# Kernel tuning notes

Hardware: AMD Instinct MI355X
Metric: run time of the kernel (lower is better)

## Reference

```python
import jax, jax.numpy as jnp
import numpy as np

B, L, H, N_OUT = 16, 2048, 256, 12
CODEBOOK_VALUE = 1.0


def setup_inputs() -> dict:
    key = jax.random.key(0)
    ks = jax.random.split(key, 7)
    s = 1.0 / np.sqrt(H)  # PyTorch default U(-1/sqrt(H), 1/sqrt(H)) init
    return {
        "embedding": jax.random.normal(ks[0], (B, L, H), jnp.float32),
        # nn.GRU(1, H): weight_ih_l0 is [3H, 1] -> store as vector [3H]
        "w_ih": jax.random.uniform(ks[1], (3 * H,), jnp.float32, -s, s),
        "w_hh": jax.random.uniform(ks[2], (3 * H, H), jnp.float32, -s, s),
        "b_ih": jax.random.uniform(ks[3], (3 * H,), jnp.float32, -s, s),
        "b_hh": jax.random.uniform(ks[4], (3 * H,), jnp.float32, -s, s),
        # nn.Linear(H, 1)
        "w_out": jax.random.uniform(ks[5], (H,), jnp.float32, -s, s),
        "b_out": jax.random.uniform(ks[6], (1,), jnp.float32, -s, s),
    }


def reference(embedding, w_ih, w_hh, b_ih, b_hh, w_out, b_out):
    Bv, Lv, Hv = embedding.shape
    e = embedding.reshape(Bv * Lv, Hv)  # [BL, H]; every step adds e to hidden

    def step(carry, _):
        h, x = carry                      # h: [BL, H], x: [BL] (quantized feedback)
        h_in = h + e                      # hidden fed to GRU is hidden_state + embedding
        # input dim is 1, so W_ih @ x reduces to outer product x * w_ih
        gi = x[:, None] * w_ih[None, :] + b_ih          # [BL, 3H]
        gh = h_in @ w_hh.T + b_hh                        # [BL, 3H]
        gi_r, gi_z, gi_n = jnp.split(gi, 3, axis=-1)     # PyTorch gate order: r, z, n
        gh_r, gh_z, gh_n = jnp.split(gh, 3, axis=-1)
        r = jax.nn.sigmoid(gi_r + gh_r)
        z = jax.nn.sigmoid(gi_z + gh_z)
        n = jnp.tanh(gi_n + r * gh_n)
        h_new = (1.0 - z) * n + z * h_in                 # GRU cell update
        o = h_new @ w_out + b_out[0]                     # [BL] output_layer
        q = jnp.where(o > 0, CODEBOOK_VALUE, -CODEBOOK_VALUE)
        return (h_new, q), (o, q)

    h0 = jnp.zeros_like(e)
    x0 = jnp.zeros((e.shape[0],), e.dtype)
    _, (outs, qs) = jax.lax.scan(step, (h0, x0), None, length=N_OUT)
    # outs/qs: [N_OUT, BL] -> [B, L, N_OUT]
    outputs = jnp.transpose(outs).reshape(Bv, Lv, N_OUT)
    quantized = jnp.transpose(qs).reshape(Bv, Lv, N_OUT)
    return outputs, quantized
```

## Files before the change

kernel.cpp:

```cpp
#include <hip/hip_runtime.h>
#include <math.h>

namespace {
constexpr int kBL = 16 * 2048;
constexpr int kH = 256;
constexpr int kNOut = 12;
constexpr int kRows = 64;
constexpr int kThreads = 1024;
constexpr int kS = 264;
constexpr int kWhh = 3 * kH * kH;
}

using short8 = __attribute__((ext_vector_type(8))) short;
using f32x4 = __attribute__((ext_vector_type(4))) float;

__device__ inline void bsplit(float v, short& h, short& l) {
  unsigned u = __float_as_uint(v);
  unsigned rh = u + 0x7FFFu + ((u >> 16) & 1u);
  h = (short)(rh >> 16);
  float hf = __uint_as_float(rh & 0xFFFF0000u);
  float r = v - hf;
  unsigned u2 = __float_as_uint(r);
  unsigned rl = u2 + 0x7FFFu + ((u2 >> 16) & 1u);
  l = (short)(rl >> 16);
}

__global__ void split_whh_kernel(const float* __restrict__ w,
                                 short* __restrict__ hi, short* __restrict__ lo) {
  const int i = (blockIdx.x * 256 + threadIdx.x) * 4;
  const float4 v = *reinterpret_cast<const float4*>(w + i);
  short4 h4, l4;
  bsplit(v.x, h4.x, l4.x);
  bsplit(v.y, h4.y, l4.y);
  bsplit(v.z, h4.z, l4.z);
  bsplit(v.w, h4.w, l4.w);
  *reinterpret_cast<short4*>(hi + i) = h4;
  *reinterpret_cast<short4*>(lo + i) = l4;
}

#define MFMA(A, B, C) __builtin_amdgcn_mfma_f32_16x16x32_bf16((A), (B), (C), 0, 0, 0)

__global__ __launch_bounds__(kThreads, 4)
void rbq_mfma3_kernel(const float* __restrict__ emb,
                      const float* __restrict__ w_ih,
                      const float* __restrict__ b_ih,
                      const float* __restrict__ b_hh,
                      const float* __restrict__ w_out,
                      const float* __restrict__ b_out,
                      const short* __restrict__ Bh,
                      const short* __restrict__ Bl,
                      float* __restrict__ out) {
  __shared__ short Ah[kRows][kS];
  __shared__ short Al[kRows][kS];
  __shared__ float osc[kRows][17];
  __shared__ float xq[kRows];

  const int tid = threadIdx.x;
  const int lane = tid & 63;
  const int wv = __builtin_amdgcn_readfirstlane(tid >> 6);
  const int grp = lane >> 4;
  const int c16 = lane & 15;
  const int row0 = blockIdx.x * kRows;
  const int j = wv * 16 + c16;

  const float wihr = w_ih[j], wihz = w_ih[kH + j], wihn = w_ih[2 * kH + j];
  const float bihr = b_ih[j], bihz = b_ih[kH + j], bihn = b_ih[2 * kH + j];
  const float bhhr = b_hh[j], bhhz = b_hh[kH + j], bhhn = b_hh[2 * kH + j];
  const float wo = w_out[j];
  const float bo = b_out[0];
  const size_t q_off = (size_t)kBL * kNOut;

  float h_reg[4][4];
#pragma unroll
  for (int m = 0; m < 4; ++m)
#pragma unroll
    for (int r = 0; r < 4; ++r) {
      const int rl = m * 16 + grp * 4 + r;
      const float e = emb[(size_t)(row0 + rl) * kH + j];
      h_reg[m][r] = e;
      short hh, hl;
      bsplit(e, hh, hl);
      Ah[rl][j] = hh;
      Al[rl][j] = hl;
    }
  if (tid < kRows) xq[tid] = 0.0f;
  __syncthreads();

  for (int step = 0; step < kNOut; ++step) {
    f32x4 acc[4][3];
#pragma unroll
    for (int m = 0; m < 4; ++m) {
      acc[m][0] = f32x4{bhhr, bhhr, bhhr, bhhr};
      acc[m][1] = f32x4{bhhz, bhhz, bhhz, bhhz};
      acc[m][2] = f32x4{bhhn, bhhn, bhhn, bhhn};
    }

#pragma unroll 1
    for (int kc = 0; kc < 8; ++kc) {
      const int ko = kc * 32 + grp * 8;
      short8 bh[3], bl[3];
#pragma unroll
      for (int g = 0; g < 3; ++g) {
        const size_t base = (size_t)(g * kH + j) * kH + ko;
        bh[g] = *reinterpret_cast<const short8*>(Bh + base);
        bl[g] = *reinterpret_cast<const short8*>(Bl + base);
      }
#pragma unroll
      for (int m = 0; m < 4; ++m) {
        const short8 ah = *reinterpret_cast<const short8*>(&Ah[m * 16 + c16][ko]);
        const short8 al = *reinterpret_cast<const short8*>(&Al[m * 16 + c16][ko]);
#pragma unroll
        for (int g = 0; g < 3; ++g) acc[m][g] = MFMA(ah, bh[g], acc[m][g]);
#pragma unroll
        for (int g = 0; g < 3; ++g) acc[m][g] = MFMA(al, bh[g], acc[m][g]);
#pragma unroll
        for (int g = 0; g < 3; ++g) acc[m][g] = MFMA(ah, bl[g], acc[m][g]);
      }
    }
    __syncthreads();

    float opart[4][4];
#pragma unroll
    for (int m = 0; m < 4; ++m) {
#pragma unroll
      for (int r = 0; r < 4; ++r) {
        const int rl = m * 16 + grp * 4 + r;
        const float x = xq[rl];
        const float ghr = acc[m][0][r];
        const float ghz = acc[m][1][r];
        const float ghn = acc[m][2][r];
        const float gr = fmaf(x, wihr, bihr) + ghr;
        const float gz = fmaf(x, wihz, bihz) + ghz;
        const float gni = fmaf(x, wihn, bihn);
        const float rg = 1.0f / (1.0f + __expf(-gr));
        const float zg = 1.0f / (1.0f + __expf(-gz));
        const float ta = gni + rg * ghn;
        const float at = fabsf(ta);
        const float et = __expf(-2.0f * at);
        const float th = copysignf((1.0f - et) / (1.0f + et), ta);
        const float hn = fmaf(zg, h_reg[m][r] - th, th);
        opart[m][r] = hn * wo;
        const float hnext = hn + emb[(size_t)(row0 + rl) * kH + j];
        h_reg[m][r] = hnext;
        short hh, hl;
        bsplit(hnext, hh, hl);
        Ah[rl][j] = hh;
        Al[rl][j] = hl;
      }
    }

#pragma unroll
    for (int m = 0; m < 4; ++m)
#pragma unroll
      for (int r = 0; r < 4; ++r) {
#pragma unroll
        for (int mask = 1; mask < 16; mask <<= 1)
          opart[m][r] += __shfl_xor(opart[m][r], mask, 16);
      }
    if (c16 == 0) {
#pragma unroll
      for (int m = 0; m < 4; ++m)
#pragma unroll
        for (int r = 0; r < 4; ++r)
          osc[m * 16 + grp * 4 + r][wv] = opart[m][r];
    }
    __syncthreads();

    if (tid < kRows) {
      float s = bo;
#pragma unroll
      for (int w2 = 0; w2 < 16; ++w2) s += osc[tid][w2];
      const float q = s > 0.0f ? 1.0f : -1.0f;
      const size_t gr = (size_t)(row0 + tid);
      out[gr * kNOut + step] = s;
      out[q_off + gr * kNOut + step] = q;
      xq[tid] = q;
    }
  }
}

extern "C" void kernel_launch(void* const* d_in, const int* in_sizes, int n_in,
                              void* d_out, int out_size, void* d_ws, size_t ws_size,
                              hipStream_t stream) {
  (void)in_sizes; (void)n_in; (void)out_size; (void)ws_size;
  const float* emb = (const float*)d_in[0];
  const float* w_ih = (const float*)d_in[1];
  const float* w_hh = (const float*)d_in[2];
  const float* b_ih = (const float*)d_in[3];
  const float* b_hh = (const float*)d_in[4];
  const float* w_out = (const float*)d_in[5];
  const float* b_out = (const float*)d_in[6];

  short* Bh = (short*)d_ws;
  short* Bl = Bh + kWhh;

  split_whh_kernel<<<kWhh / (256 * 4), 256, 0, stream>>>(w_hh, Bh, Bl);
  rbq_mfma3_kernel<<<kBL / kRows, kThreads, 0, stream>>>(
      emb, w_ih, b_ih, b_hh, w_out, b_out, Bh, Bl, (float*)d_out);
}
```

Baseline: 738.5 us.

## Double-buffer hidden-state LDS tiles to drop a barrier and broadcast feedback via shuffles

Splits the bf16 hi/lo hidden-state tiles into two ping-pong buffers. Each step then writes the next hidden state into the other buffer, which removes the barrier between the MFMA loop and the gate update. Every wave now computes the output reduction redundantly and keeps the quantized feedback in a register, read back with __shfl, so the xq shared array and one serialized tid<64 section go away. It also raises wave priority around the MFMA loop. The cost is doubled LDS usage per block, which may cut the number of resident blocks, plus redundant reduction work in every wave.

```diff
diff --git a/kernel.cpp b/kernel.cpp
--- a/kernel.cpp
+++ b/kernel.cpp
@@ -41,7 +41,7 @@
 #define MFMA(A, B, C) __builtin_amdgcn_mfma_f32_16x16x32_bf16((A), (B), (C), 0, 0, 0)
 
 __global__ __launch_bounds__(kThreads, 4)
-void rbq_mfma3_kernel(const float* __restrict__ emb,
+void rbq_mfma4_kernel(const float* __restrict__ emb,
                       const float* __restrict__ w_ih,
                       const float* __restrict__ b_ih,
                       const float* __restrict__ b_hh,
@@ -50,10 +50,9 @@
                       const short* __restrict__ Bh,
                       const short* __restrict__ Bl,
                       float* __restrict__ out) {
-  __shared__ short Ah[kRows][kS];
-  __shared__ short Al[kRows][kS];
-  __shared__ float osc[kRows][17];
-  __shared__ float xq[kRows];
+  __shared__ short Ah[2][kRows][kS];
+  __shared__ short Al[2][kRows][kS];
+  __shared__ float osc[kRows][16];
 
   const int tid = threadIdx.x;
   const int lane = tid & 63;
@@ -80,12 +79,13 @@
       h_reg[m][r] = e;
       short hh, hl;
       bsplit(e, hh, hl);
-      Ah[rl][j] = hh;
-      Al[rl][j] = hl;
-    }
-  if (tid < kRows) xq[tid] = 0.0f;
+      Ah[0][rl][j] = hh;
+      Al[0][rl][j] = hl;
+    }
+  float xqr = 0.0f;
   __syncthreads();
 
+  int p = 0;
   for (int step = 0; step < kNOut; ++step) {
     f32x4 acc[4][3];
 #pragma unroll
@@ -95,6 +95,7 @@
       acc[m][2] = f32x4{bhhn, bhhn, bhhn, bhhn};
     }
 
+    __builtin_amdgcn_s_setprio(1);
 #pragma unroll 1
     for (int kc = 0; kc < 8; ++kc) {
       const int ko = kc * 32 + grp * 8;
@@ -107,8 +108,8 @@
       }
 #pragma unroll
       for (int m = 0; m < 4; ++m) {
-        const short8 ah = *reinterpret_cast<const short8*>(&Ah[m * 16 + c16][ko]);
-        const short8 al = *reinterpret_cast<const short8*>(&Al[m * 16 + c16][ko]);
+        const short8 ah = *reinterpret_cast<const short8*>(&Ah[p][m * 16 + c16][ko]);
+        const short8 al = *reinterpret_cast<const short8*>(&Al[p][m * 16 + c16][ko]);
 #pragma unroll
         for (int g = 0; g < 3; ++g) acc[m][g] = MFMA(ah, bh[g], acc[m][g]);
 #pragma unroll
@@ -117,7 +118,7 @@
         for (int g = 0; g < 3; ++g) acc[m][g] = MFMA(ah, bl[g], acc[m][g]);
       }
     }
-    __syncthreads();
+    __builtin_amdgcn_s_setprio(0);
 
     float opart[4][4];
 #pragma unroll
@@ -125,7 +126,7 @@
 #pragma unroll
       for (int r = 0; r < 4; ++r) {
         const int rl = m * 16 + grp * 4 + r;
-        const float x = xq[rl];
+        const float x = __shfl(xqr, rl);
         const float ghr = acc[m][0][r];
         const float ghz = acc[m][1][r];
         const float ghn = acc[m][2][r];
@@ -144,8 +145,8 @@
         h_reg[m][r] = hnext;
         short hh, hl;
         bsplit(hnext, hh, hl);
-        Ah[rl][j] = hh;
-        Al[rl][j] = hl;
+        Ah[p ^ 1][rl][j] = hh;
+        Al[p ^ 1][rl][j] = hl;
       }
     }
 
@@ -166,16 +167,25 @@
     }
     __syncthreads();
 
-    if (tid < kRows) {
+    {
+      const float4 o0 = *reinterpret_cast<const float4*>(&osc[lane][0]);
+      const float4 o1 = *reinterpret_cast<const float4*>(&osc[lane][4]);
+      const float4 o2 = *reinterpret_cast<const float4*>(&osc[lane][8]);
+      const float4 o3 = *reinterpret_cast<const float4*>(&osc[lane][12]);
       float s = bo;
-#pragma unroll
-      for (int w2 = 0; w2 < 16; ++w2) s += osc[tid][w2];
+      s += o0.x; s += o0.y; s += o0.z; s += o0.w;
+      s += o1.x; s += o1.y; s += o1.z; s += o1.w;
+      s += o2.x; s += o2.y; s += o2.z; s += o2.w;
+      s += o3.x; s += o3.y; s += o3.z; s += o3.w;
       const float q = s > 0.0f ? 1.0f : -1.0f;
-      const size_t gr = (size_t)(row0 + tid);
-      out[gr * kNOut + step] = s;
-      out[q_off + gr * kNOut + step] = q;
-      xq[tid] = q;
-    }
+      xqr = q;
+      if (wv == 0) {
+        const size_t gr = (size_t)(row0 + lane);
+        out[gr * kNOut + step] = s;
+        out[q_off + gr * kNOut + step] = q;
+      }
+    }
+    p ^= 1;
   }
 }
 
@@ -195,6 +205,6 @@
   short* Bl = Bh + kWhh;
 
   split_whh_kernel<<<kWhh / (256 * 4), 256, 0, stream>>>(w_hh, Bh, Bl);
-  rbq_mfma3_kernel<<<kBL / kRows, kThreads, 0, stream>>>(
+  rbq_mfma4_kernel<<<kBL / kRows, kThreads, 0, stream>>>(
       emb, w_ih, b_ih, b_hh, w_out, b_out, Bh, Bl, (float*)d_out);
 }
```

Measured after the change: 784.2 us. +6.2%, slower.

## Software-pipeline GRU halves: overlap gate math of one half with MFMAs of other

Applied to the files above, without the earlier changes.

Halves the block to 512 threads, with each wave owning 32 hidden columns instead of 16. The 64 rows are split into two halves, and the gate nonlinearity for one half is interleaved with the MFMA matmul for the other, using double-buffered accumulators. The quantized feedback moves from shared memory into a register broadcast by shuffle, and output finalization folds into the next phase. The aim is to hide the serial gate and elementwise phase behind matrix-core work, at the cost of higher register pressure, fewer waves per block and more complex synchronization.

```diff
diff --git a/kernel.cpp b/kernel.cpp
--- a/kernel.cpp
+++ b/kernel.cpp
@@ -6,7 +6,7 @@
 constexpr int kH = 256;
 constexpr int kNOut = 12;
 constexpr int kRows = 64;
-constexpr int kThreads = 1024;
+constexpr int kThreads = 512;
 constexpr int kS = 264;
 constexpr int kWhh = 3 * kH * kH;
 }
@@ -40,8 +40,8 @@
 
 #define MFMA(A, B, C) __builtin_amdgcn_mfma_f32_16x16x32_bf16((A), (B), (C), 0, 0, 0)
 
-__global__ __launch_bounds__(kThreads, 4)
-void rbq_mfma3_kernel(const float* __restrict__ emb,
+__global__ __launch_bounds__(kThreads, 2)
+void rbq_mfma5_kernel(const float* __restrict__ emb,
                       const float* __restrict__ w_ih,
                       const float* __restrict__ b_ih,
                       const float* __restrict__ b_hh,
@@ -53,7 +53,6 @@
   __shared__ short Ah[kRows][kS];
   __shared__ short Al[kRows][kS];
   __shared__ float osc[kRows][17];
-  __shared__ float xq[kRows];
 
   const int tid = threadIdx.x;
   const int lane = tid & 63;
@@ -61,120 +60,188 @@
   const int grp = lane >> 4;
   const int c16 = lane & 15;
   const int row0 = blockIdx.x * kRows;
-  const int j = wv * 16 + c16;
-
-  const float wihr = w_ih[j], wihz = w_ih[kH + j], wihn = w_ih[2 * kH + j];
-  const float bihr = b_ih[j], bihz = b_ih[kH + j], bihn = b_ih[2 * kH + j];
-  const float bhhr = b_hh[j], bhhz = b_hh[kH + j], bhhn = b_hh[2 * kH + j];
-  const float wo = w_out[j];
+
+  float wihr[2], wihz[2], wihn[2], bihr[2], bihz[2], bihn[2];
+  float bhhr[2], bhhz[2], bhhn[2], wo[2];
+#pragma unroll
+  for (int t = 0; t < 2; ++t) {
+    const int j = wv * 32 + t * 16 + c16;
+    wihr[t] = w_ih[j]; wihz[t] = w_ih[kH + j]; wihn[t] = w_ih[2 * kH + j];
+    bihr[t] = b_ih[j]; bihz[t] = b_ih[kH + j]; bihn[t] = b_ih[2 * kH + j];
+    bhhr[t] = b_hh[j]; bhhz[t] = b_hh[kH + j]; bhhn[t] = b_hh[2 * kH + j];
+    wo[t] = w_out[j];
+  }
   const float bo = b_out[0];
   const size_t q_off = (size_t)kBL * kNOut;
 
-  float h_reg[4][4];
-#pragma unroll
-  for (int m = 0; m < 4; ++m)
-#pragma unroll
-    for (int r = 0; r < 4; ++r) {
-      const int rl = m * 16 + grp * 4 + r;
-      const float e = emb[(size_t)(row0 + rl) * kH + j];
-      h_reg[m][r] = e;
-      short hh, hl;
-      bsplit(e, hh, hl);
-      Ah[rl][j] = hh;
-      Al[rl][j] = hl;
-    }
-  if (tid < kRows) xq[tid] = 0.0f;
+  float h_reg0[2][4][2];
+  float h_reg1[2][4][2];
+#pragma unroll
+  for (int mt = 0; mt < 4; ++mt)
+#pragma unroll
+    for (int r = 0; r < 4; ++r)
+#pragma unroll
+      for (int t = 0; t < 2; ++t) {
+        const int rl = mt * 16 + grp * 4 + r;
+        const int j = wv * 32 + t * 16 + c16;
+        const float e = emb[(size_t)(row0 + rl) * kH + j];
+        if (mt < 2) h_reg0[mt][r][t] = e; else h_reg1[mt - 2][r][t] = e;
+        short hh, hl;
+        bsplit(e, hh, hl);
+        Ah[rl][j] = hh;
+        Al[rl][j] = hl;
+      }
+  float xqr = 0.0f;
   __syncthreads();
 
-  for (int step = 0; step < kNOut; ++step) {
-    f32x4 acc[4][3];
-#pragma unroll
-    for (int m = 0; m < 4; ++m) {
-      acc[m][0] = f32x4{bhhr, bhhr, bhhr, bhhr};
-      acc[m][1] = f32x4{bhhz, bhhz, bhhz, bhhz};
-      acc[m][2] = f32x4{bhhn, bhhn, bhhn, bhhn};
-    }
-
-#pragma unroll 1
+  f32x4 accA[2][2][3];
+  f32x4 accB[2][2][3];
+
+  auto phase = [&](f32x4 (&accC)[2][2][3], f32x4 (&accN)[2][2][3],
+                   float (&hreg)[2][4][2], const int mtC0, const int mtB0,
+                   const int qlo, const int outStep, const bool build,
+                   const bool gates, const bool fin) {
+    if (fin) {
+      float s = bo;
+#pragma unroll
+      for (int w2 = 0; w2 < 16; ++w2) s += osc[lane][w2];
+      const float qn = s > 0.0f ? 1.0f : -1.0f;
+      const bool inh = (lane >> 5) == (qlo >> 5);
+      xqr = inh ? qn : xqr;
+      if (wv == 0 && inh) {
+        const size_t gr = (size_t)(row0 + lane);
+        out[gr * kNOut + outStep] = s;
+        out[q_off + gr * kNOut + outStep] = qn;
+      }
+    }
+    if (build) {
+#pragma unroll
+      for (int m2 = 0; m2 < 2; ++m2)
+#pragma unroll
+        for (int t = 0; t < 2; ++t) {
+          accN[m2][t][0] = f32x4{bhhr[t], bhhr[t], bhhr[t], bhhr[t]};
+          accN[m2][t][1] = f32x4{bhhz[t], bhhz[t], bhhz[t], bhhz[t]};
+          accN[m2][t][2] = f32x4{bhhn[t], bhhn[t], bhhn[t], bhhn[t]};
+        }
+    }
+    float opart[2][4][2];
+
+    auto gate = [&](const int m2, const int r, const int t, const int rl,
+                    const float ev) {
+      const float x = __shfl(xqr, rl);
+      const float ghr = accC[m2][t][0][r];
+      const float ghz = accC[m2][t][1][r];
+      const float ghn = accC[m2][t][2][r];
+      const float gr = fmaf(x, wihr[t], bihr[t]) + ghr;
+      const float gz = fmaf(x, wihz[t], bihz[t]) + ghz;
+      const float gni = fmaf(x, wihn[t], bihn[t]);
+      const float rg = 1.0f / (1.0f + __expf(-gr));
+      const float zg = 1.0f / (1.0f + __expf(-gz));
+      const float ta = gni + rg * ghn;
+      const float at = fabsf(ta);
+      const float et = __expf(-2.0f * at);
+      const float th = copysignf((1.0f - et) / (1.0f + et), ta);
+      const float hn = fmaf(zg, hreg[m2][r][t] - th, th);
+      opart[m2][r][t] = hn * wo[t];
+      const float hnext = hn + ev;
+      hreg[m2][r][t] = hnext;
+      short hh, hl2;
+      bsplit(hnext, hh, hl2);
+      const int jj = wv * 32 + t * 16 + c16;
+      Ah[rl][jj] = hh;
+      Al[rl][jj] = hl2;
+    };
+
+#pragma unroll
     for (int kc = 0; kc < 8; ++kc) {
       const int ko = kc * 32 + grp * 8;
-      short8 bh[3], bl[3];
-#pragma unroll
-      for (int g = 0; g < 3; ++g) {
-        const size_t base = (size_t)(g * kH + j) * kH + ko;
-        bh[g] = *reinterpret_cast<const short8*>(Bh + base);
-        bl[g] = *reinterpret_cast<const short8*>(Bl + base);
-      }
-#pragma unroll
-      for (int m = 0; m < 4; ++m) {
-        const short8 ah = *reinterpret_cast<const short8*>(&Ah[m * 16 + c16][ko]);
-        const short8 al = *reinterpret_cast<const short8*>(&Al[m * 16 + c16][ko]);
-#pragma unroll
-        for (int g = 0; g < 3; ++g) acc[m][g] = MFMA(ah, bh[g], acc[m][g]);
-#pragma unroll
-        for (int g = 0; g < 3; ++g) acc[m][g] = MFMA(al, bh[g], acc[m][g]);
-#pragma unroll
-        for (int g = 0; g < 3; ++g) acc[m][g] = MFMA(ah, bl[g], acc[m][g]);
-      }
-    }
+      const int m2u = kc >> 2, ru = kc & 3;
+      const int rlu = (mtC0 + m2u) * 16 + grp * 4 + ru;
+      float e0 = 0.f, e1 = 0.f;
+      if (gates) {
+        e0 = emb[(size_t)(row0 + rlu) * kH + wv * 32 + c16];
+        e1 = emb[(size_t)(row0 + rlu) * kH + wv * 32 + 16 + c16];
+      }
+      short8 ah[2], al[2], bh[2][3], bl[2][3];
+      if (build) {
+#pragma unroll
+        for (int t = 0; t < 2; ++t)
+#pragma unroll
+          for (int g = 0; g < 3; ++g) {
+            const size_t base =
+                (size_t)(g * kH + wv * 32 + t * 16 + c16) * kH + ko;
+            bh[t][g] = *reinterpret_cast<const short8*>(Bh + base);
+            bl[t][g] = *reinterpret_cast<const short8*>(Bl + base);
+          }
+#pragma unroll
+        for (int m2 = 0; m2 < 2; ++m2) {
+          ah[m2] = *reinterpret_cast<const short8*>(&Ah[(mtB0 + m2) * 16 + c16][ko]);
+          al[m2] = *reinterpret_cast<const short8*>(&Al[(mtB0 + m2) * 16 + c16][ko]);
+        }
+#pragma unroll
+        for (int m2 = 0; m2 < 2; ++m2)
+#pragma unroll
+          for (int g = 0; g < 3; ++g) {
+            accN[m2][0][g] = MFMA(ah[m2], bh[0][g], accN[m2][0][g]);
+            accN[m2][0][g] = MFMA(al[m2], bh[0][g], accN[m2][0][g]);
+            accN[m2][0][g] = MFMA(ah[m2], bl[0][g], accN[m2][0][g]);
+          }
+      }
+      if (gates) gate(m2u, ru, 0, rlu, e0);
+      if (build) {
+#pragma unroll
+        for (int m2 = 0; m2 < 2; ++m2)
+#pragma unroll
+          for (int g = 0; g < 3; ++g) {
+            accN[m2][1][g] = MFMA(ah[m2], bh[1][g], accN[m2][1][g]);
+            accN[m2][1][g] = MFMA(al[m2], bh[1][g], accN[m2][1][g]);
+            accN[m2][1][g] = MFMA(ah[m2], bl[1][g], accN[m2][1][g]);
+          }
+      }
+      if (gates) gate(m2u, ru, 1, rlu, e1);
+    }
+
+    if (gates) {
+#pragma unroll
+      for (int m2 = 0; m2 < 2; ++m2)
+#pragma unroll
+        for (int r = 0; r < 4; ++r)
+#pragma unroll
+          for (int t = 0; t < 2; ++t) {
+#pragma unroll
+            for (int mask = 1; mask < 16; mask <<= 1)
+              opart[m2][r][t] += __shfl_xor(opart[m2][r][t], mask, 16);
+          }
+      if (c16 == 0) {
+#pragma unroll
+        for (int m2 = 0; m2 < 2; ++m2)
+#pragma unroll
+          for (int r = 0; r < 4; ++r)
+#pragma unroll
+            for (int t = 0; t < 2; ++t)
+              osc[(mtC0 + m2) * 16 + grp * 4 + r][2 * wv + t] = opart[m2][r][t];
+      }
+    }
+  };
+
+  phase(accB, accA, h_reg0, 0, 0, 0, 0, true, false, false);
+
+  for (int step = 0; step < kNOut; ++step) {
+    phase(accA, accB, h_reg0, 0, 2, 32, step - 1, true, true, step > 0);
     __syncthreads();
-
-    float opart[4][4];
-#pragma unroll
-    for (int m = 0; m < 4; ++m) {
-#pragma unroll
-      for (int r = 0; r < 4; ++r) {
-        const int rl = m * 16 + grp * 4 + r;
-        const float x = xq[rl];
-        const float ghr = acc[m][0][r];
-        const float ghz = acc[m][1][r];
-        const float ghn = acc[m][2][r];
-        const float gr = fmaf(x, wihr, bihr) + ghr;
-        const float gz = fmaf(x, wihz, bihz) + ghz;
-        const float gni = fmaf(x, wihn, bihn);
-        const float rg = 1.0f / (1.0f + __expf(-gr));
-        const float zg = 1.0f / (1.0f + __expf(-gz));
-        const float ta = gni + rg * ghn;
-        const float at = fabsf(ta);
-        const float et = __expf(-2.0f * at);
-        const float th = copysignf((1.0f - et) / (1.0f + et), ta);
-        const float hn = fmaf(zg, h_reg[m][r] - th, th);
-        opart[m][r] = hn * wo;
-        const float hnext = hn + emb[(size_t)(row0 + rl) * kH + j];
-        h_reg[m][r] = hnext;
-        short hh, hl;
-        bsplit(hnext, hh, hl);
-        Ah[rl][j] = hh;
-        Al[rl][j] = hl;
-      }
-    }
-
-#pragma unroll
-    for (int m = 0; m < 4; ++m)
-#pragma unroll
-      for (int r = 0; r < 4; ++r) {
-#pragma unroll
-        for (int mask = 1; mask < 16; mask <<= 1)
-          opart[m][r] += __shfl_xor(opart[m][r], mask, 16);
-      }
-    if (c16 == 0) {
-#pragma unroll
-      for (int m = 0; m < 4; ++m)
-#pragma unroll
-        for (int r = 0; r < 4; ++r)
-          osc[m * 16 + grp * 4 + r][wv] = opart[m][r];
-    }
+    phase(accB, accA, h_reg1, 2, 0, 0, step, step < kNOut - 1, true, true);
     __syncthreads();
-
-    if (tid < kRows) {
-      float s = bo;
-#pragma unroll
-      for (int w2 = 0; w2 < 16; ++w2) s += osc[tid][w2];
-      const float q = s > 0.0f ? 1.0f : -1.0f;
-      const size_t gr = (size_t)(row0 + tid);
-      out[gr * kNOut + step] = s;
-      out[q_off + gr * kNOut + step] = q;
-      xq[tid] = q;
+  }
+
+  {
+    float s = bo;
+#pragma unroll
+    for (int w2 = 0; w2 < 16; ++w2) s += osc[lane][w2];
+    const float qn = s > 0.0f ? 1.0f : -1.0f;
+    if (wv == 0 && lane >= 32) {
+      const size_t gr = (size_t)(row0 + lane);
+      out[gr * kNOut + (kNOut - 1)] = s;
+      out[q_off + gr * kNOut + (kNOut - 1)] = qn;
     }
   }
 }
@@ -195,6 +262,6 @@
   short* Bl = Bh + kWhh;
 
   split_whh_kernel<<<kWhh / (256 * 4), 256, 0, stream>>>(w_hh, Bh, Bl);
-  rbq_mfma3_kernel<<<kBL / kRows, kThreads, 0, stream>>>(
+  rbq_mfma5_kernel<<<kBL / kRows, kThreads, 0, stream>>>(
       emb, w_ih, b_ih, b_hh, w_out, b_out, Bh, Bl, (float*)d_out);
 }
```

Result: slower. 1.745 ms (+136.3%).

## Ping-pong two half-block warp groups to overlap MFMA and gate phases

Applied to the files above, without the earlier changes.

Splits each 1024-thread block into two 8-wave groups, each owning 32 rows. The groups alternate, so one runs the MFMA matmul while the other runs the gate math and output reduction. Gate parameters move to shared memory, the quantized feedback is kept in registers and broadcast with shuffles, and the MFMA phase raises wave priority. The aim is to hide the serial gate and reduction phase behind tensor-core work. In exchange, each wave now loads twice as many W_hh fragments per output row and the synchronisation schedule is more complex.

```diff
diff --git a/kernel.cpp b/kernel.cpp
--- a/kernel.cpp
+++ b/kernel.cpp
@@ -5,7 +5,6 @@
 constexpr int kBL = 16 * 2048;
 constexpr int kH = 256;
 constexpr int kNOut = 12;
-constexpr int kRows = 64;
 constexpr int kThreads = 1024;
 constexpr int kS = 264;
 constexpr int kWhh = 3 * kH * kH;
@@ -41,142 +40,201 @@
 #define MFMA(A, B, C) __builtin_amdgcn_mfma_f32_16x16x32_bf16((A), (B), (C), 0, 0, 0)
 
 __global__ __launch_bounds__(kThreads, 4)
-void rbq_mfma3_kernel(const float* __restrict__ emb,
-                      const float* __restrict__ w_ih,
-                      const float* __restrict__ b_ih,
-                      const float* __restrict__ b_hh,
-                      const float* __restrict__ w_out,
-                      const float* __restrict__ b_out,
-                      const short* __restrict__ Bh,
-                      const short* __restrict__ Bl,
-                      float* __restrict__ out) {
-  __shared__ short Ah[kRows][kS];
-  __shared__ short Al[kRows][kS];
-  __shared__ float osc[kRows][17];
-  __shared__ float xq[kRows];
+void rbq_pp_kernel(const float* __restrict__ emb,
+                   const float* __restrict__ w_ih,
+                   const float* __restrict__ b_ih,
+                   const float* __restrict__ b_hh,
+                   const float* __restrict__ w_out,
+                   const float* __restrict__ b_out,
+                   const short* __restrict__ Bh,
+                   const short* __restrict__ Bl,
+                   float* __restrict__ out) {
+  __shared__ short Ah[2][32][kS];
+  __shared__ short Al[2][32][kS];
+  __shared__ float prm[10][kH];
+  __shared__ float osc[2][32][12];
 
   const int tid = threadIdx.x;
   const int lane = tid & 63;
   const int wv = __builtin_amdgcn_readfirstlane(tid >> 6);
+  const int gid = wv >> 3;
+  const int gwv = wv & 7;
   const int grp = lane >> 4;
   const int c16 = lane & 15;
-  const int row0 = blockIdx.x * kRows;
-  const int j = wv * 16 + c16;
-
-  const float wihr = w_ih[j], wihz = w_ih[kH + j], wihn = w_ih[2 * kH + j];
-  const float bihr = b_ih[j], bihz = b_ih[kH + j], bihn = b_ih[2 * kH + j];
-  const float bhhr = b_hh[j], bhhz = b_hh[kH + j], bhhn = b_hh[2 * kH + j];
-  const float wo = w_out[j];
+  const int row0 = blockIdx.x * 64 + gid * 32;
+  const size_t q_off = (size_t)kBL * kNOut;
   const float bo = b_out[0];
-  const size_t q_off = (size_t)kBL * kNOut;
-
-  float h_reg[4][4];
-#pragma unroll
-  for (int m = 0; m < 4; ++m)
-#pragma unroll
-    for (int r = 0; r < 4; ++r) {
-      const int rl = m * 16 + grp * 4 + r;
-      const float e = emb[(size_t)(row0 + rl) * kH + j];
-      h_reg[m][r] = e;
-      short hh, hl;
-      bsplit(e, hh, hl);
-      Ah[rl][j] = hh;
-      Al[rl][j] = hl;
-    }
-  if (tid < kRows) xq[tid] = 0.0f;
+
+  if (tid < kH) {
+    const int u = tid;
+    prm[0][u] = w_ih[u];
+    prm[1][u] = w_ih[kH + u];
+    prm[2][u] = w_ih[2 * kH + u];
+    prm[3][u] = b_ih[u];
+    prm[4][u] = b_ih[kH + u];
+    prm[5][u] = b_ih[2 * kH + u];
+    prm[6][u] = b_hh[u];
+    prm[7][u] = b_hh[kH + u];
+    prm[8][u] = b_hh[2 * kH + u];
+    prm[9][u] = w_out[u];
+  }
+
+  float h_reg[2][4][2];
+  float xqr = 0.0f;
+#pragma unroll
+  for (int m = 0; m < 2; ++m)
+#pragma unroll
+    for (int r = 0; r < 4; ++r)
+#pragma unroll
+      for (int t = 0; t < 2; ++t) {
+        const int rl = m * 16 + grp * 4 + r;
+        const int j = gwv * 32 + t * 16 + c16;
+        const float e = emb[(size_t)(row0 + rl) * kH + j];
+        h_reg[m][r][t] = e;
+        short hh, hl;
+        bsplit(e, hh, hl);
+        Ah[gid][rl][j] = hh;
+        Al[gid][rl][j] = hl;
+      }
   __syncthreads();
 
-  for (int step = 0; step < kNOut; ++step) {
-    f32x4 acc[4][3];
-#pragma unroll
-    for (int m = 0; m < 4; ++m) {
-      acc[m][0] = f32x4{bhhr, bhhr, bhhr, bhhr};
-      acc[m][1] = f32x4{bhhz, bhhz, bhhz, bhhz};
-      acc[m][2] = f32x4{bhhn, bhhn, bhhn, bhhn};
-    }
-
+  f32x4 acc[2][2][3];
+
+  auto mfma_phase = [&]() {
+#pragma unroll
+    for (int t = 0; t < 2; ++t) {
+      const int j = gwv * 32 + t * 16 + c16;
+      const float br_ = prm[6][j], bz_ = prm[7][j], bn_ = prm[8][j];
+#pragma unroll
+      for (int m = 0; m < 2; ++m) {
+        acc[m][t][0] = f32x4{br_, br_, br_, br_};
+        acc[m][t][1] = f32x4{bz_, bz_, bz_, bz_};
+        acc[m][t][2] = f32x4{bn_, bn_, bn_, bn_};
+      }
+    }
+    __builtin_amdgcn_s_setprio(1);
 #pragma unroll 1
     for (int kc = 0; kc < 8; ++kc) {
       const int ko = kc * 32 + grp * 8;
-      short8 bh[3], bl[3];
-#pragma unroll
-      for (int g = 0; g < 3; ++g) {
-        const size_t base = (size_t)(g * kH + j) * kH + ko;
-        bh[g] = *reinterpret_cast<const short8*>(Bh + base);
-        bl[g] = *reinterpret_cast<const short8*>(Bl + base);
-      }
-#pragma unroll
-      for (int m = 0; m < 4; ++m) {
-        const short8 ah = *reinterpret_cast<const short8*>(&Ah[m * 16 + c16][ko]);
-        const short8 al = *reinterpret_cast<const short8*>(&Al[m * 16 + c16][ko]);
-#pragma unroll
-        for (int g = 0; g < 3; ++g) acc[m][g] = MFMA(ah, bh[g], acc[m][g]);
-#pragma unroll
-        for (int g = 0; g < 3; ++g) acc[m][g] = MFMA(al, bh[g], acc[m][g]);
-#pragma unroll
-        for (int g = 0; g < 3; ++g) acc[m][g] = MFMA(ah, bl[g], acc[m][g]);
-      }
-    }
-    __syncthreads();
-
-    float opart[4][4];
-#pragma unroll
-    for (int m = 0; m < 4; ++m) {
+      const short8 ah0 = *reinterpret_cast<const short8*>(&Ah[gid][c16][ko]);
+      const short8 al0 = *reinterpret_cast<const short8*>(&Al[gid][c16][ko]);
+      const short8 ah1 = *reinterpret_cast<const short8*>(&Ah[gid][16 + c16][ko]);
+      const short8 al1 = *reinterpret_cast<const short8*>(&Al[gid][16 + c16][ko]);
+#pragma unroll
+      for (int t = 0; t < 2; ++t) {
+        const int j = gwv * 32 + t * 16 + c16;
+        short8 bh[3], bl[3];
+#pragma unroll
+        for (int g = 0; g < 3; ++g) {
+          const size_t base = (size_t)(g * kH + j) * kH + ko;
+          bh[g] = *reinterpret_cast<const short8*>(Bh + base);
+          bl[g] = *reinterpret_cast<const short8*>(Bl + base);
+        }
+#pragma unroll
+        for (int g = 0; g < 3; ++g) {
+          acc[0][t][g] = MFMA(ah0, bh[g], acc[0][t][g]);
+          acc[1][t][g] = MFMA(ah1, bh[g], acc[1][t][g]);
+        }
+#pragma unroll
+        for (int g = 0; g < 3; ++g) {
+          acc[0][t][g] = MFMA(al0, bh[g], acc[0][t][g]);
+          acc[1][t][g] = MFMA(al1, bh[g], acc[1][t][g]);
+        }
+#pragma unroll
+        for (int g = 0; g < 3; ++g) {
+          acc[0][t][g] = MFMA(ah0, bl[g], acc[0][t][g]);
+          acc[1][t][g] = MFMA(ah1, bl[g], acc[1][t][g]);
+        }
+      }
+    }
+    __builtin_amdgcn_s_setprio(0);
+  };
+
+  auto gate_phase = [&]() {
+    float wr[2], wz[2], wn[2], br[2], bz[2], bn[2], wo[2];
+#pragma unroll
+    for (int t = 0; t < 2; ++t) {
+      const int j = gwv * 32 + t * 16 + c16;
+      wr[t] = prm[0][j]; wz[t] = prm[1][j]; wn[t] = prm[2][j];
+      br[t] = prm[3][j]; bz[t] = prm[4][j]; bn[t] = prm[5][j];
+      wo[t] = prm[9][j];
+    }
+    float opart[2][4];
+#pragma unroll
+    for (int m = 0; m < 2; ++m) {
 #pragma unroll
       for (int r = 0; r < 4; ++r) {
         const int rl = m * 16 + grp * 4 + r;
-        const float x = xq[rl];
-        const float ghr = acc[m][0][r];
-        const float ghz = acc[m][1][r];
-        const float ghn = acc[m][2][r];
-        const float gr = fmaf(x, wihr, bihr) + ghr;
-        const float gz = fmaf(x, wihz, bihz) + ghz;
-        const float gni = fmaf(x, wihn, bihn);
-        const float rg = 1.0f / (1.0f + __expf(-gr));
-        const float zg = 1.0f / (1.0f + __expf(-gz));
-        const float ta = gni + rg * ghn;
-        const float at = fabsf(ta);
-        const float et = __expf(-2.0f * at);
-        const float th = copysignf((1.0f - et) / (1.0f + et), ta);
-        const float hn = fmaf(zg, h_reg[m][r] - th, th);
-        opart[m][r] = hn * wo;
-        const float hnext = hn + emb[(size_t)(row0 + rl) * kH + j];
-        h_reg[m][r] = hnext;
-        short hh, hl;
-        bsplit(hnext, hh, hl);
-        Ah[rl][j] = hh;
-        Al[rl][j] = hl;
-      }
-    }
-
-#pragma unroll
-    for (int m = 0; m < 4; ++m)
-#pragma unroll
-      for (int r = 0; r < 4; ++r) {
+        const float x = __shfl(xqr, rl);
+#pragma unroll
+        for (int t = 0; t < 2; ++t) {
+          const int j = gwv * 32 + t * 16 + c16;
+          const float ghr = acc[m][t][0][r];
+          const float ghz = acc[m][t][1][r];
+          const float ghn = acc[m][t][2][r];
+          const float gr = fmaf(x, wr[t], br[t]) + ghr;
+          const float gz = fmaf(x, wz[t], bz[t]) + ghz;
+          const float gni = fmaf(x, wn[t], bn[t]);
+          const float rg = 1.0f / (1.0f + __expf(-gr));
+          const float zg = 1.0f / (1.0f + __expf(-gz));
+          const float ta = gni + rg * ghn;
+          const float at = fabsf(ta);
+          const float et = __expf(-2.0f * at);
+          const float th = copysignf((1.0f - et) / (1.0f + et), ta);
+          const float hn = fmaf(zg, h_reg[m][r][t] - th, th);
+          if (t == 0) opart[m][r] = hn * wo[0];
+          else opart[m][r] = fmaf(hn, wo[1], opart[m][r]);
+          const float hnext = hn + emb[(size_t)(row0 + rl) * kH + j];
+          h_reg[m][r][t] = hnext;
+          short hh, hl;
+          bsplit(hnext, hh, hl);
+          Ah[gid][rl][j] = hh;
+          Al[gid][rl][j] = hl;
+        }
 #pragma unroll
         for (int mask = 1; mask < 16; mask <<= 1)
           opart[m][r] += __shfl_xor(opart[m][r], mask, 16);
       }
+    }
     if (c16 == 0) {
 #pragma unroll
-      for (int m = 0; m < 4; ++m)
+      for (int m = 0; m < 2; ++m)
 #pragma unroll
         for (int r = 0; r < 4; ++r)
-          osc[m * 16 + grp * 4 + r][wv] = opart[m][r];
-    }
+          osc[gid][m * 16 + grp * 4 + r][gwv] = opart[m][r];
+    }
+  };
+
+  auto fin = [&](const int step) {
+    const int row = lane & 31;
+    const f32x4 s0 = *reinterpret_cast<const f32x4*>(&osc[gid][row][0]);
+    const f32x4 s1 = *reinterpret_cast<const f32x4*>(&osc[gid][row][4]);
+    float s = bo;
+    s += s0[0]; s += s0[1]; s += s0[2]; s += s0[3];
+    s += s1[0]; s += s1[1]; s += s1[2]; s += s1[3];
+    const float q = s > 0.0f ? 1.0f : -1.0f;
+    if (lane < 32) {
+      xqr = q;
+      if (gwv == 0) {
+        const size_t gr = (size_t)(row0 + row);
+        out[gr * kNOut + step] = s;
+        out[q_off + gr * kNOut + step] = q;
+      }
+    }
+  };
+
+  for (int k = 0; k < kNOut; ++k) {
+    if (gid == 0) { if (k > 0) fin(k - 1); mfma_phase(); }
+    else          { if (k > 0) gate_phase(); }
     __syncthreads();
-
-    if (tid < kRows) {
-      float s = bo;
-#pragma unroll
-      for (int w2 = 0; w2 < 16; ++w2) s += osc[tid][w2];
-      const float q = s > 0.0f ? 1.0f : -1.0f;
-      const size_t gr = (size_t)(row0 + tid);
-      out[gr * kNOut + step] = s;
-      out[q_off + gr * kNOut + step] = q;
-      xq[tid] = q;
-    }
+    if (gid == 0) { gate_phase(); }
+    else          { if (k > 0) fin(k - 1); mfma_phase(); }
+    __syncthreads();
   }
+  if (gid == 0) { fin(kNOut - 1); }
+  else          { gate_phase(); }
+  __syncthreads();
+  if (gid == 1) { fin(kNOut - 1); }
 }
 
 extern "C" void kernel_launch(void* const* d_in, const int* in_sizes, int n_in,
@@ -195,6 +253,6 @@
   short* Bl = Bh + kWhh;
 
   split_whh_kernel<<<kWhh / (256 * 4), 256, 0, stream>>>(w_hh, Bh, Bl);
-  rbq_mfma3_kernel<<<kBL / kRows, kThreads, 0, stream>>>(
+  rbq_pp_kernel<<<kBL / 64, kThreads, 0, stream>>>(
       emb, w_ih, b_ih, b_hh, w_out, b_out, Bh, Bl, (float*)d_out);
 }
```

Result: slower. 1.373 ms (+85.9%).
